# Kernel optimization log

Measured on AMD Instinct MI355X. Metric: run time of the kernel, lower is better.

Reference implementation:

```python
import jax, jax.numpy as jnp
import numpy as np

DIM = 384
NUM_HEADS = 6
HEAD_DIM = DIM // NUM_HEADS
MLP_HIDDEN = 4 * DIM
SCALE = HEAD_DIM ** -0.5
EPS = 1e-5


def layer_norm(x, w, b):
    mu = jnp.mean(x, axis=-1, keepdims=True)
    var = jnp.mean(jnp.square(x - mu), axis=-1, keepdims=True)
    return (x - mu) * jax.lax.rsqrt(var + EPS) * w + b


def setup_inputs() -> dict:
    key = jax.random.key(0)
    ks = jax.random.split(key, 24)
    d = DIM
    s = 0.02
    inp = {
        'x1': jax.random.normal(ks[0], (16, d, 32, 32), jnp.float32),
        'x2': jax.random.normal(ks[1], (16, d, 32, 32), jnp.float32),
        # per-branch attention-input LayerNorm + kqv projection (no bias)
        'ln_a1_w': jnp.ones((d,), jnp.float32), 'ln_a1_b': jnp.zeros((d,), jnp.float32),
        'kqv1_w': jax.random.normal(ks[2], (d, 3 * d), jnp.float32) * s,
        'ln_a2_w': jnp.ones((d,), jnp.float32), 'ln_a2_b': jnp.zeros((d,), jnp.float32),
        'kqv2_w': jax.random.normal(ks[3], (d, 3 * d), jnp.float32) * s,
        # output projections
        'proj1_w': jax.random.normal(ks[4], (d, d), jnp.float32) * s,
        'proj1_b': jnp.zeros((d,), jnp.float32),
        'proj2_w': jax.random.normal(ks[5], (d, d), jnp.float32) * s,
        'proj2_b': jnp.zeros((d,), jnp.float32),
        # post-attention LayerNorms
        'ln1_w': jnp.ones((d,), jnp.float32), 'ln1_b': jnp.zeros((d,), jnp.float32),
        'ln2_w': jnp.ones((d,), jnp.float32), 'ln2_b': jnp.zeros((d,), jnp.float32),
        # MLPs
        'mlp1_fc1_w': jax.random.normal(ks[6], (d, MLP_HIDDEN), jnp.float32) * s,
        'mlp1_fc1_b': jnp.zeros((MLP_HIDDEN,), jnp.float32),
        'mlp1_fc2_w': jax.random.normal(ks[7], (MLP_HIDDEN, d), jnp.float32) * s,
        'mlp1_fc2_b': jnp.zeros((d,), jnp.float32),
        'mlp2_fc1_w': jax.random.normal(ks[8], (d, MLP_HIDDEN), jnp.float32) * s,
        'mlp2_fc1_b': jnp.zeros((MLP_HIDDEN,), jnp.float32),
        'mlp2_fc2_w': jax.random.normal(ks[9], (MLP_HIDDEN, d), jnp.float32) * s,
        'mlp2_fc2_b': jnp.zeros((d,), jnp.float32),
    }
    return inp


def _kqv_branch(x, ln_w, ln_b, Wkqv):
    # x: [B, C, H, W] -> embedding [B, N, C]; k,q,v: [B, h, N, hd]
    B, C, H, W = x.shape
    N = H * W
    emb = x.reshape(B, C, N).transpose(0, 2, 1)
    xn = layer_norm(emb, ln_w, ln_b)
    kqv = (xn @ Wkqv).reshape(B, N, 3, NUM_HEADS, HEAD_DIM).transpose(2, 0, 3, 1, 4)
    return kqv[0], kqv[1], kqv[2], emb


def _cross_attn(q, k, v):
    # q,k,v: [B, h, N, hd] -> [B, N, C]
    scores = jnp.einsum('bhnd,bhmd->bhnm', q, k) * SCALE
    a = jax.nn.softmax(scores, axis=-1)
    o = jnp.einsum('bhnm,bhmd->bhnd', a, v)
    B, h, N, hd = o.shape
    return o.transpose(0, 2, 1, 3).reshape(B, N, h * hd)


def reference(x1, x2, ln_a1_w, ln_a1_b, kqv1_w, ln_a2_w, ln_a2_b, kqv2_w,
              proj1_w, proj1_b, proj2_w, proj2_b, ln1_w, ln1_b, ln2_w, ln2_b,
              mlp1_fc1_w, mlp1_fc1_b, mlp1_fc2_w, mlp1_fc2_b,
              mlp2_fc1_w, mlp2_fc1_b, mlp2_fc2_w, mlp2_fc2_b):
    B, C, H, W = x1.shape
    k1, q1, v1, emb1 = _kqv_branch(x1, ln_a1_w, ln_a1_b, kqv1_w)
    k2, q2, v2, emb2 = _kqv_branch(x2, ln_a2_w, ln_a2_b, kqv2_w)
    a1 = _cross_attn(q1, k2, v2)   # branch 1 queries attend to branch 2
    a2 = _cross_attn(q2, k1, v1)
    out1 = emb1 + (a1 @ proj1_w + proj1_b)
    h1 = layer_norm(out1, ln1_w, ln1_b)
    out1 = out1 + (jax.nn.gelu(h1 @ mlp1_fc1_w + mlp1_fc1_b, approximate=False) @ mlp1_fc2_w + mlp1_fc2_b)
    out2 = emb2 + (a2 @ proj2_w + proj2_b)
    h2 = layer_norm(out2, ln2_w, ln2_b)
    out2 = out2 + (jax.nn.gelu(h2 @ mlp2_fc1_w + mlp2_fc1_b, approximate=False) @ mlp2_fc2_w + mlp2_fc2_b)
    out1 = out1.transpose(0, 2, 1).reshape(B, C, H, W)
    out2 = out2.transpose(0, 2, 1).reshape(B, C, H, W)
    return (out1, out2)
```

## Files before the change

kernel.cpp:

```cpp
#include <hip/hip_runtime.h>
#include <math.h>

typedef unsigned short u16;
typedef __attribute__((ext_vector_type(8))) short short8;
typedef __attribute__((ext_vector_type(4))) short short4b;
typedef __attribute__((ext_vector_type(4))) float f32x4;

#define MFMA(a,b,c) __builtin_amdgcn_mfma_f32_16x16x32_bf16(a, b, c, 0, 0, 0)
#define SWZ(row, ch) ((((ch) ^ ((row) & 7)) << 3))
#define EXP2F(x) __builtin_amdgcn_exp2f(x)

static __device__ __forceinline__ f32x4 MFMA16(short4b a, short4b b, f32x4 c) {
#if __has_builtin(__builtin_amdgcn_mfma_f32_16x16x16bf16_1k)
    return __builtin_amdgcn_mfma_f32_16x16x16bf16_1k(a, b, c, 0, 0, 0);
#else
    f32x4 d;
    asm volatile("v_mfma_f32_16x16x16_bf16 %0, %1, %2, %3\n\ts_nop 7"
                 : "=v"(d) : "v"(a), "v"(b), "v"(c));
    return d;
#endif
}

__device__ __forceinline__ float b2f(u16 v) {
    union { unsigned int i; float f; } c; c.i = ((unsigned int)v) << 16; return c.f;
}
__device__ __forceinline__ u16 f2b(float f) {
    union { float f; unsigned int i; } c; c.f = f;
    unsigned int u = c.i;
    return (u16)((u + 0x7fffu + ((u >> 16) & 1u)) >> 16);
}
__device__ __forceinline__ u16 f2b_p(float f) {
    union { float f; unsigned int i; } c; c.f = f;
    return (u16)((c.i + 0x8000u) >> 16);
}

struct TWArgs { const float* src[8]; u16* dst[8]; int K[8]; int N[8]; };

__global__ __launch_bounds__(256) void transpose_w(TWArgs a) {
    int wi = blockIdx.z;
    int K = a.K[wi], N = a.N[wi];
    int n0 = blockIdx.x * 32, k0 = blockIdx.y * 32;
    if (n0 >= N || k0 >= K) return;
    __shared__ float t[32][33];
    const float* s = a.src[wi]; u16* d = a.dst[wi];
    int tx = threadIdx.x & 31, ty = threadIdx.x >> 5;
    for (int i = 0; i < 32; i += 8)
        t[ty + i][tx] = s[(size_t)(k0 + ty + i) * N + n0 + tx];
    __syncthreads();
    for (int i = 0; i < 32; i += 8)
        d[(size_t)(n0 + ty + i) * K + k0 + tx] = f2b(t[tx][ty + i]);
}

__global__ __launch_bounds__(256)
void ln_tr(const float* __restrict__ x0, const float* __restrict__ x1,
           const float* __restrict__ w0, const float* __restrict__ bb0,
           const float* __restrict__ w1, const float* __restrict__ bb1,
           u16* __restrict__ xn0, u16* __restrict__ xn1) {
    int br = blockIdx.z;
    const float* x  = br ? x1 : x0;
    const float* wv = br ? w1 : w0;
    const float* bv = br ? bb1 : bb0;
    u16* xn = br ? xn1 : xn0;
    int b = blockIdx.y, n0 = blockIdx.x * 32;
    __shared__ float tile[32][385];
    __shared__ float smu[32], srs[32];
    int tid = threadIdx.x;
    const float* xb = x + (size_t)b * 384 * 1024 + n0;
    for (int idx = tid; idx < 384 * 32; idx += 256) {
        int c = idx >> 5, nn = idx & 31;
        tile[nn][c] = xb[(size_t)c * 1024 + nn];
    }
    __syncthreads();
    {
        int nn = tid >> 3, part = tid & 7;
        float s1 = 0.f, s2 = 0.f;
        for (int c = part * 48; c < part * 48 + 48; ++c) {
            float v = tile[nn][c]; s1 += v; s2 += v * v;
        }
        for (int off = 1; off < 8; off <<= 1) {
            s1 += __shfl_xor(s1, off, 64); s2 += __shfl_xor(s2, off, 64);
        }
        if (part == 0) {
            float mu = s1 * (1.f / 384.f);
            float var = s2 * (1.f / 384.f) - mu * mu;
            smu[nn] = mu; srs[nn] = rsqrtf(fmaxf(var, 0.f) + 1e-5f);
        }
    }
    __syncthreads();
    size_t rowbase = (size_t)b * 1024 + n0;
    for (int idx = tid; idx < 32 * 384; idx += 256) {
        int nn = idx / 384, c = idx - nn * 384;
        float v = tile[nn][c];
        float g = (v - smu[nn]) * srs[nn] * wv[c] + bv[c];
        xn[(rowbase + nn) * 384 + c] = f2b(g);
    }
}

__global__ __launch_bounds__(256)
void ln_rows(const float* __restrict__ i0, const float* __restrict__ i1,
             const float* __restrict__ w0, const float* __restrict__ bb0,
             const float* __restrict__ w1, const float* __restrict__ bb1,
             u16* __restrict__ o0, u16* __restrict__ o1) {
    int br = blockIdx.z;
    const float* in = br ? i1 : i0;
    const float* wv = br ? w1 : w0;
    const float* bv = br ? bb1 : bb0;
    u16* out = br ? o1 : o0;
    int w = threadIdx.x >> 6, l = threadIdx.x & 63;
    size_t row = (size_t)blockIdx.x * 4 + w;
    const float* p = in + row * 384;
    float v[6]; float s1 = 0.f, s2 = 0.f;
    #pragma unroll
    for (int j = 0; j < 6; j++) { v[j] = p[j * 64 + l]; s1 += v[j]; s2 += v[j] * v[j]; }
    for (int off = 1; off < 64; off <<= 1) {
        s1 += __shfl_xor(s1, off, 64); s2 += __shfl_xor(s2, off, 64);
    }
    float mu = s1 * (1.f / 384.f);
    float var = s2 * (1.f / 384.f) - mu * mu;
    float rs = rsqrtf(fmaxf(var, 0.f) + 1e-5f);
    #pragma unroll
    for (int j = 0; j < 6; j++) {
        int c = j * 64 + l;
        out[row * 384 + c] = f2b((v[j] - mu) * rs * wv[c] + bv[c]);
    }
}

template <int EPI>
__global__ __launch_bounds__(256)
void gemm128(const u16* __restrict__ A0, const u16* __restrict__ A1,
             const u16* __restrict__ B0, const u16* __restrict__ B1,
             void* C0v, void* C1v,
             const float* __restrict__ bias0, const float* __restrict__ bias1,
             const void* R0v, const void* R1v,
             int N, int K) {
    const int br = blockIdx.z;
    const u16* A = br ? A1 : A0;
    const u16* B = br ? B1 : B0;
    void* Cv = br ? C1v : C0v;
    const float* bias = br ? bias1 : bias0;
    const void* Rv = br ? R1v : R0v;

    const int n0 = blockIdx.x * 128;
    const int m0 = blockIdx.y * 128;
    const int tid = threadIdx.x;
    const int w = tid >> 6, l = tid & 63;
    const int wm = w >> 1, wn = w & 1;
    const int lr = l & 15, lq = l >> 4;

    __shared__ alignas(16) u16 As[2][128 * 40];
    __shared__ alignas(16) u16 Bs[2][128 * 40];

    f32x4 acc[4][4];
    #pragma unroll
    for (int i = 0; i < 4; i++)
        #pragma unroll
        for (int j = 0; j < 4; j++) acc[i][j] = (f32x4)0.0f;

    const int ar0 = tid >> 2, ac0 = (tid & 3) * 8;
    const int ar1 = ar0 + 64;
    const u16* Ap0 = A + (size_t)(m0 + ar0) * K + ac0;
    const u16* Ap1 = A + (size_t)(m0 + ar1) * K + ac0;
    const u16* Bp0 = B + (size_t)(n0 + ar0) * K + ac0;
    const u16* Bp1 = B + (size_t)(n0 + ar1) * K + ac0;

    const int nk = K >> 5;
    uint4 pa0 = *(const uint4*)Ap0, pa1 = *(const uint4*)Ap1;
    uint4 pb0 = *(const uint4*)Bp0, pb1 = *(const uint4*)Bp1;
    *(uint4*)&As[0][ar0 * 40 + ac0] = pa0;
    *(uint4*)&As[0][ar1 * 40 + ac0] = pa1;
    *(uint4*)&Bs[0][ar0 * 40 + ac0] = pb0;
    *(uint4*)&Bs[0][ar1 * 40 + ac0] = pb1;
    pa0 = *(const uint4*)(Ap0 + 32); pa1 = *(const uint4*)(Ap1 + 32);
    pb0 = *(const uint4*)(Bp0 + 32); pb1 = *(const uint4*)(Bp1 + 32);
    __syncthreads();

    for (int kt = 0; kt < nk; ++kt) {
        const int cur = kt & 1;
        if (kt + 1 < nk) {
            const int nx = cur ^ 1;
            *(uint4*)&As[nx][ar0 * 40 + ac0] = pa0;
            *(uint4*)&As[nx][ar1 * 40 + ac0] = pa1;
            *(uint4*)&Bs[nx][ar0 * 40 + ac0] = pb0;
            *(uint4*)&Bs[nx][ar1 * 40 + ac0] = pb1;
        }
        if (kt + 2 < nk) {
            const int kb = (kt + 2) * 32;
            pa0 = *(const uint4*)(Ap0 + kb); pa1 = *(const uint4*)(Ap1 + kb);
            pb0 = *(const uint4*)(Bp0 + kb); pb1 = *(const uint4*)(Bp1 + kb);
        }
        short8 af[4], bf[4];
        #pragma unroll
        for (int mt = 0; mt < 4; ++mt)
            af[mt] = *(const short8*)&As[cur][(wm * 64 + mt * 16 + lr) * 40 + lq * 8];
        #pragma unroll
        for (int nt = 0; nt < 4; ++nt)
            bf[nt] = *(const short8*)&Bs[cur][(wn * 64 + nt * 16 + lr) * 40 + lq * 8];
        #pragma unroll
        for (int mt = 0; mt < 4; ++mt)
            #pragma unroll
            for (int nt = 0; nt < 4; ++nt)
                acc[mt][nt] = MFMA(af[mt], bf[nt], acc[mt][nt]);
        __syncthreads();
    }

    #pragma unroll
    for (int mt = 0; mt < 4; ++mt)
        #pragma unroll
        for (int nt = 0; nt < 4; ++nt) {
            const int col = n0 + wn * 64 + nt * 16 + lr;
            const int rbase = m0 + wm * 64 + mt * 16 + lq * 4;
            const float bv = (EPI == 0) ? 0.f : bias[col];
            #pragma unroll
            for (int r = 0; r < 4; r++) {
                const int row = rbase + r;
                const size_t idx = (size_t)row * N + col;
                float v = acc[mt][nt][r];
                if (EPI == 0) {
                    if (col < 768) {
                        ((u16*)Cv)[idx] = f2b(col >= 384 ? v * 0.18033688f : v);
                    } else {
                        u16* vtb = (u16*)Rv;
                        vtb[((((size_t)(row >> 10)) * 6 + ((col - 768) >> 6)) * 64
                             + (col & 63)) * 1024 + (row & 1023)] = f2b(v);
                    }
                } else if (EPI == 1) {
                    float xr = ((const float*)Rv)[
                        ((size_t)(row >> 10) * 384 + col) * 1024 + (row & 1023)];
                    ((float*)Cv)[idx] = v + bv + xr;
                } else if (EPI == 2) {
                    v += bv;
                    float g = 0.5f * v * (1.f + erff(v * 0.70710678118f));
                    ((u16*)Cv)[idx] = f2b(g);
                } else {
                    ((float*)Cv)[idx] = v + bv + ((const float*)Rv)[idx];
                }
            }
        }
}

__global__ __launch_bounds__(256)
void attn_k(const u16* __restrict__ kqvA, const u16* __restrict__ kqvB,
            const u16* __restrict__ vtA, const u16* __restrict__ vtB,
            u16* __restrict__ oA, u16* __restrict__ oB) {
    const int bid = blockIdx.x;
    const int g = bid & 7, qb = (bid >> 3) & 7, s = bid >> 6;
    const int grp = s * 8 + g;
    const int ob = grp & 1, h = (grp >> 1) % 6, b = grp / 12;

    const u16* kqvQ  = (ob ? kqvB : kqvA) + (size_t)b * 1024 * 1152;
    const u16* kqvKV = (ob ? kqvA : kqvB) + (size_t)b * 1024 * 1152;
    const u16* vt    = (ob ? vtA : vtB) + ((size_t)b * 6 + h) * 64 * 1024;
    u16* outp = (ob ? oB : oA) + (size_t)b * 1024 * 384;
    const u16* qp = kqvQ + 384 + h * 64;
    const u16* kp = kqvKV + h * 64;

    __shared__ alignas(16) u16 Ks[2][64 * 64];
    __shared__ alignas(16) u16 Vts[2][64 * 64];

    const int tid = threadIdx.x, w = tid >> 6, l = tid & 63;
    const int lr = l & 15, lq = l >> 4;

    short8 qf[2][2];
    #pragma unroll
    for (int a = 0; a < 2; a++)
        #pragma unroll
        for (int ks = 0; ks < 2; ks++)
            qf[a][ks] = *(const short8*)&qp[
                (size_t)(qb * 128 + w * 32 + a * 16 + lr) * 1152 + ks * 32 + lq * 8];

    const int srow = tid >> 3, sch = tid & 7;
    uint4 kpre[2][2], vpre[2][2];
    #pragma unroll
    for (int t = 0; t < 2; t++)
        #pragma unroll
        for (int i = 0; i < 2; i++) {
            int row = srow + i * 32;
            kpre[t][i] = *(const uint4*)&kp[(size_t)(t * 64 + row) * 1152 + sch * 8];
            vpre[t][i] = *(const uint4*)&vt[(size_t)row * 1024 + t * 64 + sch * 8];
        }

    #pragma unroll
    for (int i = 0; i < 2; i++) {
        int row = srow + i * 32;
        int o = row * 64 + SWZ(row, sch);
        *(uint4*)&Ks[0][o] = kpre[0][i];
        *(uint4*)&Vts[0][o] = vpre[0][i];
    }
    #pragma unroll
    for (int i = 0; i < 2; i++) {
        int row = srow + i * 32;
        kpre[0][i] = *(const uint4*)&kp[(size_t)(2 * 64 + row) * 1152 + sch * 8];
        vpre[0][i] = *(const uint4*)&vt[(size_t)row * 1024 + 2 * 64 + sch * 8];
    }

    f32x4 oacc[2][4];
    float psum[2] = {0.f, 0.f};
    #pragma unroll
    for (int a = 0; a < 2; a++)
        #pragma unroll
        for (int n = 0; n < 4; n++) oacc[a][n] = (f32x4)0.0f;

    __syncthreads();

    for (int jt = 0; jt < 16; ++jt) {
        const int cur = jt & 1, nx = cur ^ 1;
        if (jt + 1 < 16) {
            #pragma unroll
            for (int i = 0; i < 2; i++) {
                int row = srow + i * 32;
                int o = row * 64 + SWZ(row, sch);
                *(uint4*)&Ks[nx][o] = kpre[nx][i];
                *(uint4*)&Vts[nx][o] = vpre[nx][i];
            }
            if (jt + 3 < 16) {
                #pragma unroll
                for (int i = 0; i < 2; i++) {
                    int row = srow + i * 32;
                    kpre[nx][i] = *(const uint4*)&kp[(size_t)((jt + 3) * 64 + row) * 1152 + sch * 8];
                    vpre[nx][i] = *(const uint4*)&vt[(size_t)row * 1024 + (jt + 3) * 64 + sch * 8];
                }
            }
        }

        f32x4 sacc[4][2];
        #pragma unroll
        for (int kb = 0; kb < 4; kb++)
            #pragma unroll
            for (int a = 0; a < 2; a++) sacc[kb][a] = (f32x4)0.0f;
        __builtin_amdgcn_s_setprio(1);
        #pragma unroll
        for (int ks = 0; ks < 2; ++ks) {
            short8 bk[4];
            #pragma unroll
            for (int kb = 0; kb < 4; kb++) {
                int row = kb * 16 + lr;
                bk[kb] = *(const short8*)&Ks[cur][row * 64 + SWZ(row, ks * 4 + lq)];
            }
            #pragma unroll
            for (int kb = 0; kb < 4; kb++)
                #pragma unroll
                for (int a = 0; a < 2; a++)
                    sacc[kb][a] = MFMA(bk[kb], qf[a][ks], sacc[kb][a]);
        }
        __builtin_amdgcn_s_setprio(0);

        short4b ap16[2][4];
        #pragma unroll
        for (int a = 0; a < 2; a++)
            #pragma unroll
            for (int kb = 0; kb < 4; kb++) {
                f32x4 s4 = sacc[kb][a];
                float p0 = EXP2F(s4[0]), p1 = EXP2F(s4[1]);
                float p2 = EXP2F(s4[2]), p3 = EXP2F(s4[3]);
                psum[a] += (p0 + p1) + (p2 + p3);
                short4b pk;
                pk[0] = (short)f2b_p(p0); pk[1] = (short)f2b_p(p1);
                pk[2] = (short)f2b_p(p2); pk[3] = (short)f2b_p(p3);
                ap16[a][kb] = pk;
            }

        __builtin_amdgcn_s_setprio(1);
        #pragma unroll
        for (int kb = 0; kb < 4; ++kb) {
            short4b bv16[4];
            #pragma unroll
            for (int n = 0; n < 4; n++) {
                int row = n * 16 + lr;
                int addr = row * 64 + SWZ(row, kb * 2 + (lq >> 1)) + (lq & 1) * 4;
                bv16[n] = *(const short4b*)&Vts[cur][addr];
            }
            #pragma unroll
            for (int a = 0; a < 2; a++)
                #pragma unroll
                for (int n = 0; n < 4; n++)
                    oacc[a][n] = MFMA16(ap16[a][kb], bv16[n], oacc[a][n]);
        }
        __builtin_amdgcn_s_setprio(0);
        __syncthreads();
    }

    #pragma unroll
    for (int a = 0; a < 2; a++) {
        psum[a] += __shfl_xor(psum[a], 16, 64);
        psum[a] += __shfl_xor(psum[a], 32, 64);
        psum[a] = 1.f / psum[a];
    }
    float rec[2][4];
    #pragma unroll
    for (int a = 0; a < 2; a++)
        #pragma unroll
        for (int r = 0; r < 4; r++)
            rec[a][r] = __shfl(psum[a], lq * 4 + r, 64);

    #pragma unroll
    for (int a = 0; a < 2; a++)
        #pragma unroll
        for (int n = 0; n < 4; n++)
            #pragma unroll
            for (int r = 0; r < 4; r++) {
                size_t row = (size_t)qb * 128 + w * 32 + a * 16 + lq * 4 + r;
                int col = h * 64 + n * 16 + lr;
                outp[row * 384 + col] = f2b(oacc[a][n][r] * rec[a][r]);
            }
}

__global__ __launch_bounds__(256)
void transpose_out(const float* __restrict__ r0, const float* __restrict__ r1,
                   float* __restrict__ out) {
    int z = blockIdx.z, ob = z >> 4, b = z & 15;
    const float* rp = ob ? r1 : r0;
    int c0 = blockIdx.y * 32, n0 = blockIdx.x * 32;
    __shared__ float t[32][33];
    int tx = threadIdx.x & 31, ty = threadIdx.x >> 5;
    for (int i = 0; i < 32; i += 8)
        t[ty + i][tx] = rp[((size_t)b * 1024 + n0 + ty + i) * 384 + c0 + tx];
    __syncthreads();
    for (int i = 0; i < 32; i += 8)
        out[(size_t)ob * 6291456 + ((size_t)b * 384 + c0 + ty + i) * 1024 + n0 + tx]
            = t[tx][ty + i];
}

extern "C" void kernel_launch(void* const* d_in, const int* in_sizes, int n_in,
                              void* d_out, int out_size, void* d_ws, size_t ws_size,
                              hipStream_t stream) {
    const float* x1      = (const float*)d_in[0];
    const float* x2      = (const float*)d_in[1];
    const float* ln_a1_w = (const float*)d_in[2];
    const float* ln_a1_b = (const float*)d_in[3];
    const float* kqv1_w  = (const float*)d_in[4];
    const float* ln_a2_w = (const float*)d_in[5];
    const float* ln_a2_b = (const float*)d_in[6];
    const float* kqv2_w  = (const float*)d_in[7];
    const float* proj1_w = (const float*)d_in[8];
    const float* proj1_b = (const float*)d_in[9];
    const float* proj2_w = (const float*)d_in[10];
    const float* proj2_b = (const float*)d_in[11];
    const float* ln1_w   = (const float*)d_in[12];
    const float* ln1_b   = (const float*)d_in[13];
    const float* ln2_w   = (const float*)d_in[14];
    const float* ln2_b   = (const float*)d_in[15];
    const float* m1f1w   = (const float*)d_in[16];
    const float* m1f1b   = (const float*)d_in[17];
    const float* m1f2w   = (const float*)d_in[18];
    const float* m1f2b   = (const float*)d_in[19];
    const float* m2f1w   = (const float*)d_in[20];
    const float* m2f1b   = (const float*)d_in[21];
    const float* m2f2w   = (const float*)d_in[22];
    const float* m2f2b   = (const float*)d_in[23];
    (void)in_sizes; (void)n_in; (void)out_size; (void)ws_size;

    const size_t R = 16384;
    char* ws = (char*)d_ws;
    size_t off = 0;
    auto alloc = [&](size_t bytes) -> char* {
        char* p = ws + off;
        off = (off + bytes + 255) & ~(size_t)255;
        return p;
    };
    u16* kqv1t  = (u16*)alloc(1152 * 384 * 2);
    u16* kqv2t  = (u16*)alloc(1152 * 384 * 2);
    u16* proj1t = (u16*)alloc(384 * 384 * 2);
    u16* proj2t = (u16*)alloc(384 * 384 * 2);
    u16* fc11t  = (u16*)alloc(1536 * 384 * 2);
    u16* fc12t  = (u16*)alloc(1536 * 384 * 2);
    u16* fc21t  = (u16*)alloc(384 * 1536 * 2);
    u16* fc22t  = (u16*)alloc(384 * 1536 * 2);
    u16* xn1 = (u16*)alloc(R * 384 * 2);
    u16* xn2 = (u16*)alloc(R * 384 * 2);
    char* regC = alloc(R * 1152 * 2 * 2);
    u16* kqv1 = (u16*)regC;
    u16* kqv2 = (u16*)(regC + R * 1152 * 2);
    float* oa1 = (float*)regC;
    float* oa2 = (float*)(regC + R * 384 * 4);
    u16* hid_b2 = (u16*)(regC + 2 * R * 384 * 4);
    u16* at1 = (u16*)d_out;
    u16* at2 = at1 + R * 384;
    u16* vt1 = at2 + R * 384;
    u16* vt2 = vt1 + (size_t)16 * 6 * 64 * 1024;
    u16* hid_b1 = (u16*)d_out;

    TWArgs tw;
    tw.src[0] = kqv1_w;  tw.dst[0] = kqv1t;  tw.K[0] = 384;  tw.N[0] = 1152;
    tw.src[1] = kqv2_w;  tw.dst[1] = kqv2t;  tw.K[1] = 384;  tw.N[1] = 1152;
    tw.src[2] = proj1_w; tw.dst[2] = proj1t; tw.K[2] = 384;  tw.N[2] = 384;
    tw.src[3] = proj2_w; tw.dst[3] = proj2t; tw.K[3] = 384;  tw.N[3] = 384;
    tw.src[4] = m1f1w;   tw.dst[4] = fc11t;  tw.K[4] = 384;  tw.N[4] = 1536;
    tw.src[5] = m2f1w;   tw.dst[5] = fc12t;  tw.K[5] = 384;  tw.N[5] = 1536;
    tw.src[6] = m1f2w;   tw.dst[6] = fc21t;  tw.K[6] = 1536; tw.N[6] = 384;
    tw.src[7] = m2f2w;   tw.dst[7] = fc22t;  tw.K[7] = 1536; tw.N[7] = 384;
    transpose_w<<<dim3(48, 48, 8), dim3(256), 0, stream>>>(tw);

    ln_tr<<<dim3(32, 16, 2), dim3(256), 0, stream>>>(
        x1, x2, ln_a1_w, ln_a1_b, ln_a2_w, ln_a2_b, xn1, xn2);

    gemm128<0><<<dim3(9, 128, 2), dim3(256), 0, stream>>>(
        xn1, xn2, kqv1t, kqv2t, (void*)kqv1, (void*)kqv2,
        (const float*)nullptr, (const float*)nullptr,
        (const void*)vt1, (const void*)vt2, 1152, 384);

    attn_k<<<dim3(1536), dim3(256), 0, stream>>>(kqv1, kqv2, vt1, vt2, at1, at2);

    gemm128<1><<<dim3(3, 128, 2), dim3(256), 0, stream>>>(
        at1, at2, proj1t, proj2t, (void*)oa1, (void*)oa2,
        proj1_b, proj2_b, (const void*)x1, (const void*)x2, 384, 384);

    ln_rows<<<dim3(4096, 1, 2), dim3(256), 0, stream>>>(
        oa1, oa2, ln1_w, ln1_b, ln2_w, ln2_b, xn1, xn2);

    for (int half = 0; half < 2; ++half) {
        const size_t ro = (size_t)half * 8192;
        gemm128<2><<<dim3(12, 64, 2), dim3(256), 0, stream>>>(
            xn1 + ro * 384, xn2 + ro * 384, fc11t, fc12t,
            (void*)hid_b1, (void*)hid_b2, m1f1b, m2f1b, nullptr, nullptr, 1536, 384);
        gemm128<3><<<dim3(3, 64, 2), dim3(256), 0, stream>>>(
            hid_b1, hid_b2, fc21t, fc22t,
            (void*)(oa1 + ro * 384), (void*)(oa2 + ro * 384),
            m1f2b, m2f2b, (const void*)(oa1 + ro * 384), (const void*)(oa2 + ro * 384),
            384, 1536);
    }

    transpose_out<<<dim3(32, 12, 32), dim3(256), 0, stream>>>(oa1, oa2, (float*)d_out);
}
```

Baseline: 623.5 us.

## Use direct global-to-LDS loads in GEMM and vectorize LayerNorm transpose I/O

After: 628.3 us. About the same (+0.8%).

```diff
diff --git a/kernel.cpp b/kernel.cpp
--- a/kernel.cpp
+++ b/kernel.cpp
@@ -19,6 +19,12 @@
                  : "=v"(d) : "v"(a), "v"(b), "v"(c));
     return d;
 #endif
+}
+
+__device__ __forceinline__ void gload_lds16(const u16* g, u16* l) {
+    __builtin_amdgcn_global_load_lds(
+        (const __attribute__((address_space(1))) unsigned int*)(const void*)g,
+        (__attribute__((address_space(3))) unsigned int*)(void*)l, 16, 0, 0);
 }
 
 __device__ __forceinline__ float b2f(u16 v) {
@@ -66,9 +72,11 @@
     __shared__ float smu[32], srs[32];
     int tid = threadIdx.x;
     const float* xb = x + (size_t)b * 384 * 1024 + n0;
-    for (int idx = tid; idx < 384 * 32; idx += 256) {
-        int c = idx >> 5, nn = idx & 31;
-        tile[nn][c] = xb[(size_t)c * 1024 + nn];
+    for (int idx = tid; idx < 384 * 8; idx += 256) {
+        int c = idx >> 3, q = idx & 7;
+        const float4 v = *(const float4*)&xb[(size_t)c * 1024 + q * 4];
+        tile[q * 4 + 0][c] = v.x; tile[q * 4 + 1][c] = v.y;
+        tile[q * 4 + 2][c] = v.z; tile[q * 4 + 3][c] = v.w;
     }
     __syncthreads();
     {
@@ -88,11 +96,16 @@
     }
     __syncthreads();
     size_t rowbase = (size_t)b * 1024 + n0;
-    for (int idx = tid; idx < 32 * 384; idx += 256) {
-        int nn = idx / 384, c = idx - nn * 384;
-        float v = tile[nn][c];
-        float g = (v - smu[nn]) * srs[nn] * wv[c] + bv[c];
-        xn[(rowbase + nn) * 384 + c] = f2b(g);
+    for (int idx = tid; idx < 1536; idx += 256) {
+        int nn = idx / 48, c0 = (idx - nn * 48) * 8;
+        float mu = smu[nn], rs = srs[nn];
+        u16 ov[8];
+        #pragma unroll
+        for (int k = 0; k < 8; k++) {
+            int c = c0 + k;
+            ov[k] = f2b((tile[nn][c] - mu) * rs * wv[c] + bv[c]);
+        }
+        *(uint4*)&xn[(rowbase + nn) * 384 + c0] = *(uint4*)ov;
     }
 }
 
@@ -147,8 +160,8 @@
     const int wm = w >> 1, wn = w & 1;
     const int lr = l & 15, lq = l >> 4;
 
-    __shared__ alignas(16) u16 As[2][128 * 40];
-    __shared__ alignas(16) u16 Bs[2][128 * 40];
+    __shared__ alignas(16) u16 As[2][128 * 32];
+    __shared__ alignas(16) u16 Bs[2][128 * 32];
 
     f32x4 acc[4][4];
     #pragma unroll
@@ -156,45 +169,40 @@
         #pragma unroll
         for (int j = 0; j < 4; j++) acc[i][j] = (f32x4)0.0f;
 
-    const int ar0 = tid >> 2, ac0 = (tid & 3) * 8;
-    const int ar1 = ar0 + 64;
-    const u16* Ap0 = A + (size_t)(m0 + ar0) * K + ac0;
-    const u16* Ap1 = A + (size_t)(m0 + ar1) * K + ac0;
-    const u16* Bp0 = B + (size_t)(n0 + ar0) * K + ac0;
-    const u16* Bp1 = B + (size_t)(n0 + ar1) * K + ac0;
+    const int idx0 = w * 128 + l;
+    const int row0 = idx0 >> 2, ch0 = (idx0 & 3) * 8;
+    const int idx1 = idx0 + 64;
+    const int row1 = idx1 >> 2, ch1 = (idx1 & 3) * 8;
+    const u16* Asrc0 = A + (size_t)(m0 + row0) * K + ch0;
+    const u16* Asrc1 = A + (size_t)(m0 + row1) * K + ch1;
+    const u16* Bsrc0 = B + (size_t)(n0 + row0) * K + ch0;
+    const u16* Bsrc1 = B + (size_t)(n0 + row1) * K + ch1;
+    const int ldsoff0 = (w * 2 + 0) * 512, ldsoff1 = (w * 2 + 1) * 512;
 
     const int nk = K >> 5;
-    uint4 pa0 = *(const uint4*)Ap0, pa1 = *(const uint4*)Ap1;
-    uint4 pb0 = *(const uint4*)Bp0, pb1 = *(const uint4*)Bp1;
-    *(uint4*)&As[0][ar0 * 40 + ac0] = pa0;
-    *(uint4*)&As[0][ar1 * 40 + ac0] = pa1;
-    *(uint4*)&Bs[0][ar0 * 40 + ac0] = pb0;
-    *(uint4*)&Bs[0][ar1 * 40 + ac0] = pb1;
-    pa0 = *(const uint4*)(Ap0 + 32); pa1 = *(const uint4*)(Ap1 + 32);
-    pb0 = *(const uint4*)(Bp0 + 32); pb1 = *(const uint4*)(Bp1 + 32);
+    gload_lds16(Asrc0, &As[0][ldsoff0]);
+    gload_lds16(Asrc1, &As[0][ldsoff1]);
+    gload_lds16(Bsrc0, &Bs[0][ldsoff0]);
+    gload_lds16(Bsrc1, &Bs[0][ldsoff1]);
     __syncthreads();
 
     for (int kt = 0; kt < nk; ++kt) {
         const int cur = kt & 1;
         if (kt + 1 < nk) {
             const int nx = cur ^ 1;
-            *(uint4*)&As[nx][ar0 * 40 + ac0] = pa0;
-            *(uint4*)&As[nx][ar1 * 40 + ac0] = pa1;
-            *(uint4*)&Bs[nx][ar0 * 40 + ac0] = pb0;
-            *(uint4*)&Bs[nx][ar1 * 40 + ac0] = pb1;
-        }
-        if (kt + 2 < nk) {
-            const int kb = (kt + 2) * 32;
-            pa0 = *(const uint4*)(Ap0 + kb); pa1 = *(const uint4*)(Ap1 + kb);
-            pb0 = *(const uint4*)(Bp0 + kb); pb1 = *(const uint4*)(Bp1 + kb);
+            const int kb = (kt + 1) * 32;
+            gload_lds16(Asrc0 + kb, &As[nx][ldsoff0]);
+            gload_lds16(Asrc1 + kb, &As[nx][ldsoff1]);
+            gload_lds16(Bsrc0 + kb, &Bs[nx][ldsoff0]);
+            gload_lds16(Bsrc1 + kb, &Bs[nx][ldsoff1]);
         }
         short8 af[4], bf[4];
         #pragma unroll
         for (int mt = 0; mt < 4; ++mt)
-            af[mt] = *(const short8*)&As[cur][(wm * 64 + mt * 16 + lr) * 40 + lq * 8];
+            af[mt] = *(const short8*)&As[cur][(wm * 64 + mt * 16 + lr) * 32 + lq * 8];
         #pragma unroll
         for (int nt = 0; nt < 4; ++nt)
-            bf[nt] = *(const short8*)&Bs[cur][(wn * 64 + nt * 16 + lr) * 40 + lq * 8];
+            bf[nt] = *(const short8*)&Bs[cur][(wn * 64 + nt * 16 + lr) * 32 + lq * 8];
         #pragma unroll
         for (int mt = 0; mt < 4; ++mt)
             #pragma unroll
```
